# Optimization experiments

Measured on AMD Instinct MI355X. Metric: run time of the kernel, lower is better.

## Reference

```python
import jax, jax.numpy as jnp
import numpy as np

N = 50000
D = 1024
EPS = 1e-5

def gcn(x, W, b, src, dst, n):
    # PyG GCNConv: h = x @ W; add self-loops; symmetric normalization.
    h = x @ W
    deg = jnp.zeros((n,), h.dtype).at[dst].add(1.0) + 1.0  # +1 for self-loop
    dinv = jax.lax.rsqrt(deg)
    norm = dinv[src] * dinv[dst]                  # [E]
    agg = jnp.zeros_like(h).at[dst].add(h[src] * norm[:, None])
    agg = agg + h * (dinv * dinv)[:, None]        # self-loop contribution
    return agg + b

def bn(x, g, bt, m, v):
    # eval-mode BatchNorm1d with running stats
    return (x - m) * jax.lax.rsqrt(v + EPS) * g + bt

def branch(x, ei, W1, b1, g1, bt1, m1, v1, W2, b2, g2, bt2, m2, v2, W3, b3, g3, bt3, m3, v3):
    src, dst = ei[0], ei[1]
    h = jax.nn.relu(bn(gcn(x, W1, b1, src, dst, N), g1, bt1, m1, v1))
    h = jax.nn.relu(bn(gcn(h, W2, b2, src, dst, N), g2, bt2, m2, v2))
    emb = bn(gcn(h, W3, b3, src, dst, N), g3, bt3, m3, v3)   # node embeddings, no relu
    return jnp.mean(emb, axis=0, keepdims=True)              # [1, 64] global mean pool

def setup_inputs() -> dict:
    key = jax.random.key(0)
    ks = iter(jax.random.split(key, 64))
    inp = {}
    for i, nm in enumerate(['x0', 'x1', 'x2']):
        inp[nm] = jax.random.normal(next(ks), (N, D), jnp.float32)
    for nm, e in [('ei0', 150000), ('ei1', 300000), ('ei2', 600000)]:
        inp[nm] = jax.random.randint(next(ks), (2, e), 0, N, jnp.int64)
    dims = [(D, 256, '1'), (256, 128, '2'), (128, 64, '3')]
    for din, dout, s in dims:
        inp['W' + s + 's'] = jax.random.normal(next(ks), (3, din, dout), jnp.float32) * 0.02
        inp['B' + s + 's'] = jax.random.normal(next(ks), (3, dout), jnp.float32) * 0.02
        inp['g' + s + 's'] = jax.random.uniform(next(ks), (3, dout), jnp.float32, 0.5, 1.5)
        inp['bt' + s + 's'] = jax.random.normal(next(ks), (3, dout), jnp.float32) * 0.02
        inp['m' + s + 's'] = jax.random.normal(next(ks), (3, dout), jnp.float32) * 0.02
        inp['v' + s + 's'] = jax.random.uniform(next(ks), (3, dout), jnp.float32, 0.5, 1.5)
    inp['fuse_W'] = jax.random.normal(next(ks), (192, 64), jnp.float32) * 0.05
    inp['fuse_b'] = jax.random.normal(next(ks), (64,), jnp.float32) * 0.02
    inp['cls_W'] = jax.random.normal(next(ks), (64, 10), jnp.float32) * 0.1
    inp['cls_b'] = jax.random.normal(next(ks), (10,), jnp.float32) * 0.02
    inp['reg_W'] = jax.random.normal(next(ks), (64, 1), jnp.float32) * 0.1
    inp['reg_b'] = jax.random.normal(next(ks), (1,), jnp.float32) * 0.02
    return inp

def reference(x0, x1, x2, ei0, ei1, ei2,
              W1s, B1s, g1s, bt1s, m1s, v1s,
              W2s, B2s, g2s, bt2s, m2s, v2s,
              W3s, B3s, g3s, bt3s, m3s, v3s,
              fuse_W, fuse_b, cls_W, cls_b, reg_W, reg_b):
    xs = [x0, x1, x2]
    eis = [ei0, ei1, ei2]
    embs = []
    for s in range(3):  # fixed small loop over scales (different edge counts)
        embs.append(branch(xs[s], eis[s],
                           W1s[s], B1s[s], g1s[s], bt1s[s], m1s[s], v1s[s],
                           W2s[s], B2s[s], g2s[s], bt2s[s], m2s[s], v2s[s],
                           W3s[s], B3s[s], g3s[s], bt3s[s], m3s[s], v3s[s]))
    fused = jax.nn.relu(jnp.concatenate(embs, axis=-1) @ fuse_W + fuse_b)  # [1, 64]
    classification = fused @ cls_W + cls_b                                  # [1, 10]
    regression = jax.nn.sigmoid(fused @ reg_W + reg_b)                      # [1, 1]
    return (classification, regression)
```

## Files before the change

kernel.cpp:

```cpp
#include <hip/hip_runtime.h>
#include <cstdint>
#include <cstddef>

#define NNODES 50000

typedef __attribute__((ext_vector_type(8))) short short8;
typedef __attribute__((ext_vector_type(4))) float f32x4;
typedef __attribute__((ext_vector_type(4))) unsigned short u16x4;
typedef __attribute__((ext_vector_type(2))) unsigned short u16x2;
typedef __attribute__((ext_vector_type(4))) unsigned int u32x4;

__device__ __forceinline__ unsigned short f2bf(float f) {
  unsigned u = __builtin_bit_cast(unsigned, f);
  u = u + 0x7FFFu + ((u >> 16) & 1u);
  return (unsigned short)(u >> 16);
}
__device__ __forceinline__ float bf2f(unsigned short u) {
  return __builtin_bit_cast(float, (unsigned)u << 16);
}
__device__ __forceinline__ unsigned cvtpk(float lo, float hi) {
  unsigned r;
  asm("v_cvt_pk_bf16_f32 %0, %1, %2" : "=v"(r) : "v"(lo), "v"(hi));
  return r;
}

__global__ void deg_count3_kernel(const int* __restrict__ e0, const int* __restrict__ e1,
                                  const int* __restrict__ e2, int E0, int E1, int E2,
                                  int* __restrict__ deg, int n) {
  int s = blockIdx.y;
  const int* ei = s == 0 ? e0 : (s == 1 ? e1 : e2);
  int E = s == 0 ? E0 : (s == 1 ? E1 : E2);
  int i = blockIdx.x * blockDim.x + threadIdx.x;
  if (i < E) atomicAdd(&deg[(size_t)s * n + ei[E + i]], 1);
}

__global__ void deg_finish_kernel(const int* __restrict__ deg, float* __restrict__ dinv, int n) {
  int i = blockIdx.x * blockDim.x + threadIdx.x;
  if (i < n) dinv[i] = rsqrtf((float)deg[i] + 1.0f);
}

__global__ void csum_count3_kernel(const int* __restrict__ e0, const int* __restrict__ e1,
                                   const int* __restrict__ e2, int E0, int E1, int E2,
                                   const float* __restrict__ dinv_all, float* __restrict__ csum,
                                   int n) {
  int s = blockIdx.y;
  const int* ei = s == 0 ? e0 : (s == 1 ? e1 : e2);
  int E = s == 0 ? E0 : (s == 1 ? E1 : E2);
  int i = blockIdx.x * blockDim.x + threadIdx.x;
  if (i < E)
    unsafeAtomicAdd(&csum[(size_t)s * n + ei[i]], dinv_all[(size_t)s * n + ei[E + i]]);
}

__global__ void c_finish_kernel(const float* __restrict__ dinv, float* __restrict__ csum, int n) {
  int i = blockIdx.x * blockDim.x + threadIdx.x;
  if (i < n) csum[i] = dinv[i] * (dinv[i] + csum[i]);
}

__global__ void bsum_kernel(const int* __restrict__ deg, int* __restrict__ bsum, int n,
                            int nchunk) {
  int s = blockIdx.y, c = blockIdx.x;
  int i = c * 256 + threadIdx.x;
  int v = (i < n) ? deg[(size_t)s * n + i] : 0;
  __shared__ int red[256];
  red[threadIdx.x] = v;
  __syncthreads();
  for (int o = 128; o > 0; o >>= 1) {
    if (threadIdx.x < o) red[threadIdx.x] += red[threadIdx.x + o];
    __syncthreads();
  }
  if (threadIdx.x == 0) bsum[s * nchunk + c] = red[0];
}

__global__ void bscan_kernel(int* __restrict__ bsum, int nchunk) {
  int s = blockIdx.x;
  __shared__ int tmp[256];
  int v = (threadIdx.x < nchunk) ? bsum[s * nchunk + threadIdx.x] : 0;
  tmp[threadIdx.x] = v;
  __syncthreads();
  for (int o = 1; o < 256; o <<= 1) {
    int t = (threadIdx.x >= o) ? tmp[threadIdx.x - o] : 0;
    __syncthreads();
    tmp[threadIdx.x] += t;
    __syncthreads();
  }
  if (threadIdx.x < nchunk) bsum[s * nchunk + threadIdx.x] = tmp[threadIdx.x] - v;
}

__global__ void rowptr_kernel(const int* __restrict__ deg, const int* __restrict__ bsum,
                              int* __restrict__ rowptr, int* __restrict__ cursor, int n,
                              int nchunk) {
  int s = blockIdx.y, c = blockIdx.x;
  int i = c * 256 + threadIdx.x;
  int v = (i < n) ? deg[(size_t)s * n + i] : 0;
  __shared__ int tmp[256];
  tmp[threadIdx.x] = v;
  __syncthreads();
  for (int o = 1; o < 256; o <<= 1) {
    int t = (threadIdx.x >= o) ? tmp[threadIdx.x - o] : 0;
    __syncthreads();
    tmp[threadIdx.x] += t;
    __syncthreads();
  }
  int incl = tmp[threadIdx.x] + bsum[s * nchunk + c];
  if (i < n) {
    rowptr[(size_t)s * (n + 1) + i + 1] = incl;
    cursor[(size_t)s * n + i] = incl - v;
  }
  if (i == 0) rowptr[(size_t)s * (n + 1)] = 0;
}

__global__ void csr_fill3_kernel(const int* __restrict__ e0, const int* __restrict__ e1,
                                 const int* __restrict__ e2, int E0, int E1, int E2,
                                 int* __restrict__ cursor, int* __restrict__ csr, int n) {
  int s = blockIdx.y;
  const int* ei = s == 0 ? e0 : (s == 1 ? e1 : e2);
  int E = s == 0 ? E0 : (s == 1 ? E1 : E2);
  int coff = (s > 0 ? E0 : 0) + (s > 1 ? E1 : 0);
  int i = blockIdx.x * blockDim.x + threadIdx.x;
  if (i < E) {
    int src = ei[i];
    int dst = ei[E + i];
    int pos = atomicAdd(&cursor[(size_t)s * n + dst], 1);
    csr[coff + pos] = src;
  }
}

__global__ void wt_all_kernel(const float* __restrict__ W0, const float* __restrict__ W1,
                              unsigned short* __restrict__ Wt) {
  int idx = blockIdx.x * blockDim.x + threadIdx.x;
  const int L0TOT = 3 * 262144;
  const int TOT = L0TOT + 3 * 32768;
  if (idx >= TOT) return;
  if (idx < L0TOT) {
    int s = idx / 262144, r = idx - s * 262144;
    int n = r >> 10, k = r & 1023;
    Wt[idx] = f2bf(W0[(size_t)s * 262144 + k * 256 + n]);
  } else {
    int j = idx - L0TOT;
    int s = j / 32768, r = j - s * 32768;
    int n = r >> 8, k = r & 255;
    Wt[idx] = f2bf(W1[(size_t)s * 32768 + k * 128 + n]);
  }
}

template <int A_FP32, int WR, int WC, int NT>
__global__ __launch_bounds__(NT) void gemm_lds3_kernel(
    const void* __restrict__ A0v, const void* __restrict__ A1v, const void* __restrict__ A2v,
    const unsigned short* __restrict__ Wt, int wtStride,
    unsigned short* __restrict__ H, size_t hStride,
    const float* __restrict__ dinv_all, int M, int K, int Nc) {
  constexpr int BM = WR * 64;
  constexpr int BN = WC * 64;
  constexpr int ABYTES = BM * 64 * (A_FP32 ? 4 : 2);
  constexpr int BBYTES = BN * 64 * 2;
  constexpr int AISS = ABYTES / (16 * NT);
  constexpr int BISS = BBYTES / (16 * NT);

  __shared__ unsigned char lds[ABYTES + BBYTES];
  float* AldsF = (float*)lds;
  unsigned short* AldsH = (unsigned short*)lds;
  unsigned short* Blds = (unsigned short*)(lds + ABYTES);

  const int sc = blockIdx.y;
  const void* Av = sc == 0 ? A0v : (sc == 1 ? A1v : A2v);
  const unsigned short* Wts = Wt + (size_t)sc * wtStride;
  unsigned short* Hs = H + (size_t)sc * hStride;
  const float* dinv = dinv_all + (size_t)sc * M;
  const int tid = threadIdx.x;
  const int lane = tid & 63;
  const int w = tid >> 6;
  const int wr = w / WC;
  const int wc = w - wr * WC;
  const int r0 = blockIdx.x * BM;
  const float* Af = (const float*)Av;
  const unsigned short* Ab = (const unsigned short*)Av;
  const int NT16 = K >> 6;

  f32x4 acc[4][4] = {};

  for (int t = 0; t < NT16; ++t) {
    const int k0 = t << 6;
#pragma unroll
    for (int i = 0; i < AISS; i++) {
      int c = (w * AISS + i) * 64 + lane;
      if constexpr (A_FP32) {
        int row = c >> 4, j = c & 15;
        int gr = r0 + row;
        if (gr > M - 1) gr = M - 1;
        const float* src = Af + (size_t)gr * K + k0 + ((j ^ (row & 7)) << 2);
        __builtin_amdgcn_global_load_lds(
            (const __attribute__((address_space(1))) void*)src,
            (__attribute__((address_space(3))) void*)(lds + (size_t)(w * AISS + i) * 1024),
            16, 0, 0);
      } else {
        int row = c >> 3, j = c & 7;
        int gr = r0 + row;
        if (gr > M - 1) gr = M - 1;
        const unsigned short* src = Ab + (size_t)gr * K + k0 + ((j ^ (row & 7)) << 3);
        __builtin_amdgcn_global_load_lds(
            (const __attribute__((address_space(1))) void*)src,
            (__attribute__((address_space(3))) void*)(lds + (size_t)(w * AISS + i) * 1024),
            16, 0, 0);
      }
    }
#pragma unroll
    for (int i = 0; i < BISS; i++) {
      int c = (w * BISS + i) * 64 + lane;
      int n = c >> 3, j = c & 7;
      const unsigned short* src = Wts + (size_t)n * K + k0 + ((j ^ (n & 7)) << 3);
      __builtin_amdgcn_global_load_lds(
          (const __attribute__((address_space(1))) void*)src,
          (__attribute__((address_space(3))) void*)(lds + ABYTES + (size_t)(w * BISS + i) * 1024),
          16, 0, 0);
    }
    __syncthreads();

#pragma unroll
    for (int kk = 0; kk < 2; kk++) {
      const int t16 = kk * 4 + (lane >> 4);
      short8 af[4], bfr[4];
#pragma unroll
      for (int mi = 0; mi < 4; mi++) {
        int row = wr * 64 + mi * 16 + (lane & 15);
        if constexpr (A_FP32) {
          const float* bp = AldsF + row * 64;
          f32x4 u0 = *(const f32x4*)(bp + ((((2 * t16)) ^ (row & 7)) << 2));
          f32x4 u1 = *(const f32x4*)(bp + (((2 * t16 + 1) ^ (row & 7)) << 2));
          u32x4 p;
          p[0] = cvtpk(u0[0], u0[1]);
          p[1] = cvtpk(u0[2], u0[3]);
          p[2] = cvtpk(u1[0], u1[1]);
          p[3] = cvtpk(u1[2], u1[3]);
          af[mi] = __builtin_bit_cast(short8, p);
        } else {
          af[mi] = *(const short8*)(AldsH + row * 64 + ((t16 ^ (row & 7)) << 3));
        }
      }
#pragma unroll
      for (int ni = 0; ni < 4; ni++) {
        int n = wc * 64 + ni * 16 + (lane & 15);
        bfr[ni] = *(const short8*)(Blds + n * 64 + ((t16 ^ (n & 7)) << 3));
      }
#pragma unroll
      for (int mi = 0; mi < 4; mi++)
#pragma unroll
        for (int ni = 0; ni < 4; ni++)
          acc[mi][ni] =
              __builtin_amdgcn_mfma_f32_16x16x32_bf16(af[mi], bfr[ni], acc[mi][ni], 0, 0, 0);
    }
    __syncthreads();
  }

#pragma unroll
  for (int mi = 0; mi < 4; mi++) {
#pragma unroll
    for (int r = 0; r < 4; r++) {
      int gr = r0 + wr * 64 + mi * 16 + (lane >> 4) * 4 + r;
      if (gr < M) {
        float di = dinv[gr];
#pragma unroll
        for (int ni = 0; ni < 4; ni++) {
          int col = wc * 64 + ni * 16 + (lane & 15);
          Hs[(size_t)gr * Nc + col] = f2bf(acc[mi][ni][r] * di);
        }
      }
    }
  }
}

template <int VEC>
__device__ __forceinline__ void addrow(const unsigned short* __restrict__ p, float* acc) {
  if constexpr (VEC == 4) {
    u16x4 u = *(const u16x4*)p;
#pragma unroll
    for (int j = 0; j < 4; j++) acc[j] += bf2f(u[j]);
  } else {
    u16x2 u = *(const u16x2*)p;
    acc[0] += bf2f(u[0]);
    acc[1] += bf2f(u[1]);
  }
}

template <int VEC>
__global__ __launch_bounds__(256) void agg3_kernel(
    const unsigned short* __restrict__ Hb, size_t hStride,
    const int* __restrict__ rowptr, const int* __restrict__ csr, int E0, int E1,
    const float* __restrict__ dinv_all,
    const float* __restrict__ Bb, const float* __restrict__ g,
    const float* __restrict__ bt, const float* __restrict__ m,
    const float* __restrict__ v, unsigned short* __restrict__ X, size_t xStride, int n) {
  const int C = VEC * 64;
  const int sIdx = blockIdx.y;
  const unsigned short* Hs = Hb + (size_t)sIdx * hStride;
  unsigned short* Xs = X + (size_t)sIdx * xStride;
  const int* rp = rowptr + (size_t)sIdx * (n + 1);
  const int* cs = csr + (sIdx > 0 ? E0 : 0) + (sIdx > 1 ? E1 : 0);
  const float* dinv = dinv_all + (size_t)sIdx * n;
  const int lane = threadIdx.x & 63;
  const int w = threadIdx.x >> 6;
  const int ch = lane * VEC;
  float a[VEC], sh[VEC];
#pragma unroll
  for (int j = 0; j < VEC; j++) {
    float aa = g[sIdx * C + ch + j] * rsqrtf(v[sIdx * C + ch + j] + 1e-5f);
    a[j] = aa;
    sh[j] = (Bb[sIdx * C + ch + j] - m[sIdx * C + ch + j]) * aa + bt[sIdx * C + ch + j];
  }
  const int row = blockIdx.x * 4 + w;
  if (row >= n) return;
  float acc[VEC] = {};
  addrow<VEC>(Hs + (size_t)row * C + ch, acc);
  int b0 = rp[row], b1 = rp[row + 1];
  int i = b0;
  for (; i + 8 <= b1; i += 8) {
    int s0 = cs[i], s1 = cs[i + 1], s2 = cs[i + 2], s3 = cs[i + 3];
    int s4 = cs[i + 4], s5 = cs[i + 5], s6 = cs[i + 6], s7 = cs[i + 7];
    addrow<VEC>(Hs + (size_t)s0 * C + ch, acc);
    addrow<VEC>(Hs + (size_t)s1 * C + ch, acc);
    addrow<VEC>(Hs + (size_t)s2 * C + ch, acc);
    addrow<VEC>(Hs + (size_t)s3 * C + ch, acc);
    addrow<VEC>(Hs + (size_t)s4 * C + ch, acc);
    addrow<VEC>(Hs + (size_t)s5 * C + ch, acc);
    addrow<VEC>(Hs + (size_t)s6 * C + ch, acc);
    addrow<VEC>(Hs + (size_t)s7 * C + ch, acc);
  }
  for (; i < b1; i++) addrow<VEC>(Hs + (size_t)cs[i] * C + ch, acc);
  float dd = dinv[row];
  if constexpr (VEC == 4) {
    u16x4 o;
#pragma unroll
    for (int j = 0; j < 4; j++) o[j] = f2bf(fmaxf(acc[j] * dd * a[j] + sh[j], 0.0f));
    *(u16x4*)(Xs + (size_t)row * C + ch) = o;
  } else {
    u16x2 o;
    o[0] = f2bf(fmaxf(acc[0] * dd * a[0] + sh[0], 0.0f));
    o[1] = f2bf(fmaxf(acc[1] * dd * a[1] + sh[1], 0.0f));
    *(u16x2*)(Xs + (size_t)row * C + ch) = o;
  }
}

__global__ __launch_bounds__(256) void colsum3_kernel(const unsigned short* __restrict__ X,
                                                      size_t xStride,
                                                      const float* __restrict__ c_all,
                                                      float* __restrict__ pooled, int n) {
  const int s = blockIdx.y;
  const unsigned short* Xs = X + (size_t)s * xStride;
  const float* c = c_all + (size_t)s * n;
  const int ch = threadIdx.x & 127;
  const int half = threadIdx.x >> 7;
  float acc = 0.0f;
  for (int row = blockIdx.x * 2 + half; row < n; row += gridDim.x * 2)
    acc += c[row] * bf2f(Xs[(size_t)row * 128 + ch]);
  __shared__ float red[256];
  red[threadIdx.x] = acc;
  __syncthreads();
  if (threadIdx.x < 128)
    unsafeAtomicAdd(&pooled[s * 128 + ch], red[threadIdx.x] + red[threadIdx.x + 128]);
}

__global__ void head_kernel(const float* __restrict__ pooled, const float* __restrict__ W3p,
                            const float* __restrict__ B3p, const float* __restrict__ g3p,
                            const float* __restrict__ bt3p, const float* __restrict__ m3p,
                            const float* __restrict__ v3p, const float* __restrict__ fuse_W,
                            const float* __restrict__ fuse_b, const float* __restrict__ cls_W,
                            const float* __restrict__ cls_b, const float* __restrict__ reg_W,
                            const float* __restrict__ reg_b, float* __restrict__ out) {
  __shared__ float e[192];
  __shared__ float fused[64];
  int t = threadIdx.x;
  if (t < 192) {
    int s = t >> 6, ch = t & 63;
    float acc = 0.0f;
    const float* W3 = W3p + (size_t)s * 128 * 64;
    const float* pv = pooled + s * 128;
    for (int k = 0; k < 128; k++) acc += pv[k] * W3[k * 64 + ch];
    float a3 = g3p[s * 64 + ch] * rsqrtf(v3p[s * 64 + ch] + 1e-5f);
    e[t] = (acc * (1.0f / (float)NNODES) + B3p[s * 64 + ch] - m3p[s * 64 + ch]) * a3 +
           bt3p[s * 64 + ch];
  }
  __syncthreads();
  if (t < 64) {
    float acc = fuse_b[t];
    for (int k = 0; k < 192; k++) acc += e[k] * fuse_W[k * 64 + t];
    fused[t] = fmaxf(acc, 0.0f);
  }
  __syncthreads();
  if (t < 10) {
    float acc = cls_b[t];
    for (int k = 0; k < 64; k++) acc += fused[k] * cls_W[k * 10 + t];
    out[t] = acc;
  }
  if (t == 64) {
    float acc = reg_b[0];
    for (int k = 0; k < 64; k++) acc += fused[k] * reg_W[k];
    out[10] = 1.0f / (1.0f + expf(-acc));
  }
}

extern "C" void kernel_launch(void* const* d_in, const int* in_sizes, int n_in,
                              void* d_out, int out_size, void* d_ws, size_t ws_size,
                              hipStream_t stream) {
  const int N = NNODES;
  const int NCHUNK = (N + 255) / 256;
  const float* xs[3] = {(const float*)d_in[0], (const float*)d_in[1], (const float*)d_in[2]};
  const int* eis[3] = {(const int*)d_in[3], (const int*)d_in[4], (const int*)d_in[5]};
  int Es[3];
  for (int s = 0; s < 3; s++) Es[s] = in_sizes[3 + s] / 2;
  int maxE = Es[0] > Es[1] ? Es[0] : Es[1];
  if (Es[2] > maxE) maxE = Es[2];

  const float* Wp[2]  = {(const float*)d_in[6],  (const float*)d_in[12]};
  const float* Bp[2]  = {(const float*)d_in[7],  (const float*)d_in[13]};
  const float* gp[2]  = {(const float*)d_in[8],  (const float*)d_in[14]};
  const float* btp[2] = {(const float*)d_in[9],  (const float*)d_in[15]};
  const float* mp[2]  = {(const float*)d_in[10], (const float*)d_in[16]};
  const float* vp[2]  = {(const float*)d_in[11], (const float*)d_in[17]};
  const float* W3p  = (const float*)d_in[18];
  const float* B3p  = (const float*)d_in[19];
  const float* g3p  = (const float*)d_in[20];
  const float* bt3p = (const float*)d_in[21];
  const float* m3p  = (const float*)d_in[22];
  const float* v3p  = (const float*)d_in[23];
  const float* fuse_W = (const float*)d_in[24];
  const float* fuse_b = (const float*)d_in[25];
  const float* cls_W  = (const float*)d_in[26];
  const float* cls_b  = (const float*)d_in[27];
  const float* reg_W  = (const float*)d_in[28];
  const float* reg_b  = (const float*)d_in[29];

  size_t off = 0;
  auto alloc = [&](size_t nbytes) {
    char* p = (char*)d_ws + off;
    off += (nbytes + 255) & ~(size_t)255;
    return (void*)p;
  };
  int*   deg      = (int*)alloc(3 * (size_t)N * 4);
  float* dinv_all = (float*)alloc(3 * (size_t)N * 4);
  float* c_all    = (float*)alloc(3 * (size_t)N * 4);
  float* pooled   = (float*)alloc(3 * 128 * 4);
  int*   bsum     = (int*)alloc(3 * (size_t)NCHUNK * 4);
  int*   rowptr   = (int*)alloc(3 * (size_t)(N + 1) * 4);
  int*   cursor   = (int*)alloc(3 * (size_t)N * 4);
  int*   csr      = (int*)alloc((size_t)(Es[0] + Es[1] + Es[2]) * 4);
  unsigned short* Hbuf = (unsigned short*)alloc(3 * (size_t)N * 256 * 2);
  unsigned short* Xbf  = (unsigned short*)alloc(3 * (size_t)N * 256 * 2);
  unsigned short* Wt   = (unsigned short*)alloc((size_t)(3 * 262144 + 3 * 32768) * 2);
  (void)ws_size; (void)n_in; (void)out_size;

  const size_t HS = (size_t)N * 256;

  hipMemsetAsync(deg, 0, 3 * (size_t)N * 4, stream);
  hipMemsetAsync(c_all, 0, 3 * (size_t)N * 4, stream);
  hipMemsetAsync(pooled, 0, 3 * 128 * 4, stream);

  dim3 eg((maxE + 255) / 256, 3);
  deg_count3_kernel<<<eg, 256, 0, stream>>>(eis[0], eis[1], eis[2], Es[0], Es[1], Es[2], deg, N);
  deg_finish_kernel<<<(3 * N + 255) / 256, 256, 0, stream>>>(deg, dinv_all, 3 * N);
  csum_count3_kernel<<<eg, 256, 0, stream>>>(eis[0], eis[1], eis[2], Es[0], Es[1], Es[2],
                                             dinv_all, c_all, N);
  c_finish_kernel<<<(3 * N + 255) / 256, 256, 0, stream>>>(dinv_all, c_all, 3 * N);
  bsum_kernel<<<dim3(NCHUNK, 3), 256, 0, stream>>>(deg, bsum, N, NCHUNK);
  bscan_kernel<<<3, 256, 0, stream>>>(bsum, NCHUNK);
  rowptr_kernel<<<dim3(NCHUNK, 3), 256, 0, stream>>>(deg, bsum, rowptr, cursor, N, NCHUNK);
  csr_fill3_kernel<<<eg, 256, 0, stream>>>(eis[0], eis[1], eis[2], Es[0], Es[1], Es[2], cursor,
                                           csr, N);
  wt_all_kernel<<<(3 * 262144 + 3 * 32768 + 255) / 256, 256, 0, stream>>>(Wp[0], Wp[1], Wt);

  gemm_lds3_kernel<1, 2, 4, 512><<<dim3((N + 127) / 128, 3), 512, 0, stream>>>(
      xs[0], xs[1], xs[2], Wt, 262144, Hbuf, HS, dinv_all, N, 1024, 256);
  agg3_kernel<4><<<dim3((N + 3) / 4, 3), 256, 0, stream>>>(
      Hbuf, HS, rowptr, csr, Es[0], Es[1], dinv_all, Bp[0], gp[0], btp[0], mp[0], vp[0], Xbf,
      HS, N);

  gemm_lds3_kernel<0, 2, 2, 256><<<dim3((N + 127) / 128, 3), 256, 0, stream>>>(
      Xbf, Xbf + HS, Xbf + 2 * HS, Wt + 3 * 262144, 32768, Hbuf, HS, dinv_all, N, 256, 128);
  agg3_kernel<2><<<dim3((N + 3) / 4, 3), 256, 0, stream>>>(
      Hbuf, HS, rowptr, csr, Es[0], Es[1], dinv_all, Bp[1], gp[1], btp[1], mp[1], vp[1], Xbf,
      HS, N);

  colsum3_kernel<<<dim3(512, 3), 256, 0, stream>>>(Xbf, HS, c_all, pooled, N);

  head_kernel<<<1, 192, 0, stream>>>(pooled, W3p, B3p, g3p, bt3p, m3p, v3p, fuse_W, fuse_b,
                                     cls_W, cls_b, reg_W, reg_b, (float*)d_out);
}
```

Baseline: 712.5 us.

## Double-buffer LDS tiles in GEMM to overlap global loads with MFMA

```diff
diff --git a/kernel.cpp b/kernel.cpp
--- a/kernel.cpp
+++ b/kernel.cpp
@@ -143,23 +143,23 @@
   }
 }
 
-template <int A_FP32, int WR, int WC, int NT>
-__global__ __launch_bounds__(NT) void gemm_lds3_kernel(
+template <int A_FP32, int WR, int WC, int NT, int KDIM>
+__global__ __launch_bounds__(NT) void gemm_pipe3_kernel(
     const void* __restrict__ A0v, const void* __restrict__ A1v, const void* __restrict__ A2v,
     const unsigned short* __restrict__ Wt, int wtStride,
     unsigned short* __restrict__ H, size_t hStride,
-    const float* __restrict__ dinv_all, int M, int K, int Nc) {
+    const float* __restrict__ dinv_all, int M, int Nc) {
   constexpr int BM = WR * 64;
   constexpr int BN = WC * 64;
   constexpr int ABYTES = BM * 64 * (A_FP32 ? 4 : 2);
   constexpr int BBYTES = BN * 64 * 2;
+  constexpr int TILEB = ABYTES + BBYTES;
   constexpr int AISS = ABYTES / (16 * NT);
   constexpr int BISS = BBYTES / (16 * NT);
-
-  __shared__ unsigned char lds[ABYTES + BBYTES];
-  float* AldsF = (float*)lds;
-  unsigned short* AldsH = (unsigned short*)lds;
-  unsigned short* Blds = (unsigned short*)(lds + ABYTES);
+  constexpr int ISS = AISS + BISS;
+  constexpr int NTILES = KDIM / 64;
+
+  __shared__ unsigned char lds[2 * TILEB];
 
   const int sc = blockIdx.y;
   const void* Av = sc == 0 ? A0v : (sc == 1 ? A1v : A2v);
@@ -174,12 +174,10 @@
   const int r0 = blockIdx.x * BM;
   const float* Af = (const float*)Av;
   const unsigned short* Ab = (const unsigned short*)Av;
-  const int NT16 = K >> 6;
-
-  f32x4 acc[4][4] = {};
-
-  for (int t = 0; t < NT16; ++t) {
+
+  auto issueTile = [&](int t, int buf) {
     const int k0 = t << 6;
+    unsigned char* ldsb = lds + (size_t)buf * TILEB;
 #pragma unroll
     for (int i = 0; i < AISS; i++) {
       int c = (w * AISS + i) * 64 + lane;
@@ -187,19 +185,19 @@
         int row = c >> 4, j = c & 15;
         int gr = r0 + row;
         if (gr > M - 1) gr = M - 1;
-        const float* src = Af + (size_t)gr * K + k0 + ((j ^ (row & 7)) << 2);
+        const float* src = Af + (size_t)gr * KDIM + k0 + ((j ^ (row & 7)) << 2);
         __builtin_amdgcn_global_load_lds(
             (const __attribute__((address_space(1))) void*)src,
-            (__attribute__((address_space(3))) void*)(lds + (size_t)(w * AISS + i) * 1024),
+            (__attribute__((address_space(3))) void*)(ldsb + (size_t)(w * AISS + i) * 1024),
             16, 0, 0);
       } else {
         int row = c >> 3, j = c & 7;
         int gr = r0 + row;
         if (gr > M - 1) gr = M - 1;
-        const unsigned short* src = Ab + (size_t)gr * K + k0 + ((j ^ (row & 7)) << 3);
+        const unsigned short* src = Ab + (size_t)gr * KDIM + k0 + ((j ^ (row & 7)) << 3);
         __builtin_amdgcn_global_load_lds(
             (const __attribute__((address_space(1))) void*)src,
-            (__attribute__((address_space(3))) void*)(lds + (size_t)(w * AISS + i) * 1024),
+            (__attribute__((address_space(3))) void*)(ldsb + (size_t)(w * AISS + i) * 1024),
             16, 0, 0);
       }
     }
@@ -207,14 +205,22 @@
     for (int i = 0; i < BISS; i++) {
       int c = (w * BISS + i) * 64 + lane;
       int n = c >> 3, j = c & 7;
-      const unsigned short* src = Wts + (size_t)n * K + k0 + ((j ^ (n & 7)) << 3);
+      const unsigned short* src = Wts + (size_t)n * KDIM + k0 + ((j ^ (n & 7)) << 3);
       __builtin_amdgcn_global_load_lds(
           (const __attribute__((address_space(1))) void*)src,
-          (__attribute__((address_space(3))) void*)(lds + ABYTES + (size_t)(w * BISS + i) * 1024),
+          (__attribute__((address_space(3))) void*)(ldsb + ABYTES +
+                                                    (size_t)(w * BISS + i) * 1024),
           16, 0, 0);
     }
-    __syncthreads();
-
+  };
+
+  f32x4 acc[4][4] = {};
+
+  auto computeT = [&](int buf) {
+    const float* AldsF = (const float*)(lds + (size_t)buf * TILEB);
+    const unsigned short* AldsH = (const unsigned short*)(lds + (size_t)buf * TILEB);
+    const unsigned short* Blds =
+        (const unsigned short*)(lds + (size_t)buf * TILEB + ABYTES);
 #pragma unroll
     for (int kk = 0; kk < 2; kk++) {
       const int t16 = kk * 4 + (lane >> 4);
@@ -248,8 +254,21 @@
           acc[mi][ni] =
               __builtin_amdgcn_mfma_f32_16x16x32_bf16(af[mi], bfr[ni], acc[mi][ni], 0, 0, 0);
     }
-    __syncthreads();
-  }
+  };
+
+  issueTile(0, 0);
+  issueTile(1, 1);
+#pragma unroll 1
+  for (int t = 0; t < NTILES - 1; ++t) {
+    asm volatile("s_waitcnt vmcnt(%0)" ::"n"(ISS) : "memory");
+    asm volatile("s_barrier" ::: "memory");
+    computeT(t & 1);
+    asm volatile("s_waitcnt lgkmcnt(0)\ns_barrier" ::: "memory");
+    if (t + 2 < NTILES) issueTile(t + 2, t & 1);
+  }
+  asm volatile("s_waitcnt vmcnt(0)" ::: "memory");
+  asm volatile("s_barrier" ::: "memory");
+  computeT((NTILES - 1) & 1);
 
 #pragma unroll
   for (int mi = 0; mi < 4; mi++) {
@@ -466,14 +485,14 @@
                                            csr, N);
   wt_all_kernel<<<(3 * 262144 + 3 * 32768 + 255) / 256, 256, 0, stream>>>(Wp[0], Wp[1], Wt);
 
-  gemm_lds3_kernel<1, 2, 4, 512><<<dim3((N + 127) / 128, 3), 512, 0, stream>>>(
-      xs[0], xs[1], xs[2], Wt, 262144, Hbuf, HS, dinv_all, N, 1024, 256);
+  gemm_pipe3_kernel<1, 2, 4, 512, 1024><<<dim3((N + 127) / 128, 3), 512, 0, stream>>>(
+      xs[0], xs[1], xs[2], Wt, 262144, Hbuf, HS, dinv_all, N, 256);
   agg3_kernel<4><<<dim3((N + 3) / 4, 3), 256, 0, stream>>>(
       Hbuf, HS, rowptr, csr, Es[0], Es[1], dinv_all, Bp[0], gp[0], btp[0], mp[0], vp[0], Xbf,
       HS, N);
 
-  gemm_lds3_kernel<0, 2, 2, 256><<<dim3((N + 127) / 128, 3), 256, 0, stream>>>(
-      Xbf, Xbf + HS, Xbf + 2 * HS, Wt + 3 * 262144, 32768, Hbuf, HS, dinv_all, N, 256, 128);
+  gemm_pipe3_kernel<0, 2, 2, 256, 256><<<dim3((N + 127) / 128, 3), 256, 0, stream>>>(
+      Xbf, Xbf + HS, Xbf + 2 * HS, Wt + 3 * 262144, 32768, Hbuf, HS, dinv_all, N, 128);
   agg3_kernel<2><<<dim3((N + 3) / 4, 3), 256, 0, stream>>>(
       Hbuf, HS, rowptr, csr, Es[0], Es[1], dinv_all, Bp[1], gp[1], btp[1], mp[1], vp[1], Xbf,
       HS, N);
```

New measurement: 676.5 us. 1.05x faster.

## Fuse weighted column-sum pooling into layer-2 aggregation and retile first GEMM

Applied to the files above, without the earlier changes.

```diff
diff --git a/kernel.cpp b/kernel.cpp
--- a/kernel.cpp
+++ b/kernel.cpp
@@ -281,14 +281,15 @@
   }
 }
 
-template <int VEC>
+template <int VEC, int POOL>
 __global__ __launch_bounds__(256) void agg3_kernel(
     const unsigned short* __restrict__ Hb, size_t hStride,
     const int* __restrict__ rowptr, const int* __restrict__ csr, int E0, int E1,
     const float* __restrict__ dinv_all,
     const float* __restrict__ Bb, const float* __restrict__ g,
     const float* __restrict__ bt, const float* __restrict__ m,
-    const float* __restrict__ v, unsigned short* __restrict__ X, size_t xStride, int n) {
+    const float* __restrict__ v, unsigned short* __restrict__ X, size_t xStride,
+    const float* __restrict__ c_all, float* __restrict__ pooled_rep, int n) {
   const int C = VEC * 64;
   const int sIdx = blockIdx.y;
   const unsigned short* Hs = Hb + (size_t)sIdx * hStride;
@@ -296,6 +297,7 @@
   const int* rp = rowptr + (size_t)sIdx * (n + 1);
   const int* cs = csr + (sIdx > 0 ? E0 : 0) + (sIdx > 1 ? E1 : 0);
   const float* dinv = dinv_all + (size_t)sIdx * n;
+  const float* cw = c_all + (size_t)sIdx * n;
   const int lane = threadIdx.x & 63;
   const int w = threadIdx.x >> 6;
   const int ch = lane * VEC;
@@ -306,74 +308,83 @@
     a[j] = aa;
     sh[j] = (Bb[sIdx * C + ch + j] - m[sIdx * C + ch + j]) * aa + bt[sIdx * C + ch + j];
   }
-  const int row = blockIdx.x * 4 + w;
-  if (row >= n) return;
-  float acc[VEC] = {};
-  addrow<VEC>(Hs + (size_t)row * C + ch, acc);
-  int b0 = rp[row], b1 = rp[row + 1];
-  int i = b0;
-  for (; i + 8 <= b1; i += 8) {
-    int s0 = cs[i], s1 = cs[i + 1], s2 = cs[i + 2], s3 = cs[i + 3];
-    int s4 = cs[i + 4], s5 = cs[i + 5], s6 = cs[i + 6], s7 = cs[i + 7];
-    addrow<VEC>(Hs + (size_t)s0 * C + ch, acc);
-    addrow<VEC>(Hs + (size_t)s1 * C + ch, acc);
-    addrow<VEC>(Hs + (size_t)s2 * C + ch, acc);
-    addrow<VEC>(Hs + (size_t)s3 * C + ch, acc);
-    addrow<VEC>(Hs + (size_t)s4 * C + ch, acc);
-    addrow<VEC>(Hs + (size_t)s5 * C + ch, acc);
-    addrow<VEC>(Hs + (size_t)s6 * C + ch, acc);
-    addrow<VEC>(Hs + (size_t)s7 * C + ch, acc);
-  }
-  for (; i < b1; i++) addrow<VEC>(Hs + (size_t)cs[i] * C + ch, acc);
-  float dd = dinv[row];
-  if constexpr (VEC == 4) {
-    u16x4 o;
-#pragma unroll
-    for (int j = 0; j < 4; j++) o[j] = f2bf(fmaxf(acc[j] * dd * a[j] + sh[j], 0.0f));
-    *(u16x4*)(Xs + (size_t)row * C + ch) = o;
-  } else {
-    u16x2 o;
-    o[0] = f2bf(fmaxf(acc[0] * dd * a[0] + sh[0], 0.0f));
-    o[1] = f2bf(fmaxf(acc[1] * dd * a[1] + sh[1], 0.0f));
-    *(u16x2*)(Xs + (size_t)row * C + ch) = o;
-  }
-}
-
-__global__ __launch_bounds__(256) void colsum3_kernel(const unsigned short* __restrict__ X,
-                                                      size_t xStride,
-                                                      const float* __restrict__ c_all,
-                                                      float* __restrict__ pooled, int n) {
-  const int s = blockIdx.y;
-  const unsigned short* Xs = X + (size_t)s * xStride;
-  const float* c = c_all + (size_t)s * n;
-  const int ch = threadIdx.x & 127;
-  const int half = threadIdx.x >> 7;
-  float acc = 0.0f;
-  for (int row = blockIdx.x * 2 + half; row < n; row += gridDim.x * 2)
-    acc += c[row] * bf2f(Xs[(size_t)row * 128 + ch]);
-  __shared__ float red[256];
-  red[threadIdx.x] = acc;
-  __syncthreads();
-  if (threadIdx.x < 128)
-    unsafeAtomicAdd(&pooled[s * 128 + ch], red[threadIdx.x] + red[threadIdx.x + 128]);
-}
-
-__global__ void head_kernel(const float* __restrict__ pooled, const float* __restrict__ W3p,
+  float pool[VEC] = {};
+  const int stride = gridDim.x * 4;
+  for (int row = blockIdx.x * 4 + w; row < n; row += stride) {
+    float acc[VEC] = {};
+    addrow<VEC>(Hs + (size_t)row * C + ch, acc);
+    int b0 = rp[row], b1 = rp[row + 1];
+    int i = b0;
+    for (; i + 8 <= b1; i += 8) {
+      int s0 = cs[i], s1 = cs[i + 1], s2 = cs[i + 2], s3 = cs[i + 3];
+      int s4 = cs[i + 4], s5 = cs[i + 5], s6 = cs[i + 6], s7 = cs[i + 7];
+      addrow<VEC>(Hs + (size_t)s0 * C + ch, acc);
+      addrow<VEC>(Hs + (size_t)s1 * C + ch, acc);
+      addrow<VEC>(Hs + (size_t)s2 * C + ch, acc);
+      addrow<VEC>(Hs + (size_t)s3 * C + ch, acc);
+      addrow<VEC>(Hs + (size_t)s4 * C + ch, acc);
+      addrow<VEC>(Hs + (size_t)s5 * C + ch, acc);
+      addrow<VEC>(Hs + (size_t)s6 * C + ch, acc);
+      addrow<VEC>(Hs + (size_t)s7 * C + ch, acc);
+    }
+    for (; i < b1; i++) addrow<VEC>(Hs + (size_t)cs[i] * C + ch, acc);
+    float dd = dinv[row];
+    if constexpr (!POOL) {
+      if constexpr (VEC == 4) {
+        u16x4 o;
+#pragma unroll
+        for (int j = 0; j < 4; j++) o[j] = f2bf(fmaxf(acc[j] * dd * a[j] + sh[j], 0.0f));
+        *(u16x4*)(Xs + (size_t)row * C + ch) = o;
+      } else {
+        u16x2 o;
+        o[0] = f2bf(fmaxf(acc[0] * dd * a[0] + sh[0], 0.0f));
+        o[1] = f2bf(fmaxf(acc[1] * dd * a[1] + sh[1], 0.0f));
+        *(u16x2*)(Xs + (size_t)row * C + ch) = o;
+      }
+    } else {
+      float cr = cw[row];
+#pragma unroll
+      for (int j = 0; j < VEC; j++)
+        pool[j] += cr * fmaxf(acc[j] * dd * a[j] + sh[j], 0.0f);
+    }
+  }
+  if constexpr (POOL) {
+    __shared__ float red[4 * 128];
+#pragma unroll
+    for (int j = 0; j < VEC; j++) red[w * 128 + ch + j] = pool[j];
+    __syncthreads();
+    int t = threadIdx.x;
+    if (t < 128) {
+      float val = red[t] + red[128 + t] + red[256 + t] + red[384 + t];
+      unsafeAtomicAdd(&pooled_rep[(((size_t)(blockIdx.x & 7) * 3 + sIdx) << 7) + t], val);
+    }
+  }
+}
+
+__global__ void head_kernel(const float* __restrict__ pooled_rep, const float* __restrict__ W3p,
                             const float* __restrict__ B3p, const float* __restrict__ g3p,
                             const float* __restrict__ bt3p, const float* __restrict__ m3p,
                             const float* __restrict__ v3p, const float* __restrict__ fuse_W,
                             const float* __restrict__ fuse_b, const float* __restrict__ cls_W,
                             const float* __restrict__ cls_b, const float* __restrict__ reg_W,
                             const float* __restrict__ reg_b, float* __restrict__ out) {
+  __shared__ float pv[3 * 128];
   __shared__ float e[192];
   __shared__ float fused[64];
   int t = threadIdx.x;
+  for (int idx = t; idx < 384; idx += 192) {
+    int s = idx >> 7, k = idx & 127;
+    float acc = 0.0f;
+#pragma unroll
+    for (int r = 0; r < 8; r++) acc += pooled_rep[((r * 3 + s) << 7) + k];
+    pv[idx] = acc;
+  }
+  __syncthreads();
   if (t < 192) {
     int s = t >> 6, ch = t & 63;
     float acc = 0.0f;
     const float* W3 = W3p + (size_t)s * 128 * 64;
-    const float* pv = pooled + s * 128;
-    for (int k = 0; k < 128; k++) acc += pv[k] * W3[k * 64 + ch];
+    for (int k = 0; k < 128; k++) acc += pv[s * 128 + k] * W3[k * 64 + ch];
     float a3 = g3p[s * 64 + ch] * rsqrtf(v3p[s * 64 + ch] + 1e-5f);
     e[t] = (acc * (1.0f / (float)NNODES) + B3p[s * 64 + ch] - m3p[s * 64 + ch]) * a3 +
            bt3p[s * 64 + ch];
@@ -434,14 +445,14 @@
     off += (nbytes + 255) & ~(size_t)255;
     return (void*)p;
   };
-  int*   deg      = (int*)alloc(3 * (size_t)N * 4);
-  float* dinv_all = (float*)alloc(3 * (size_t)N * 4);
-  float* c_all    = (float*)alloc(3 * (size_t)N * 4);
-  float* pooled   = (float*)alloc(3 * 128 * 4);
-  int*   bsum     = (int*)alloc(3 * (size_t)NCHUNK * 4);
-  int*   rowptr   = (int*)alloc(3 * (size_t)(N + 1) * 4);
-  int*   cursor   = (int*)alloc(3 * (size_t)N * 4);
-  int*   csr      = (int*)alloc((size_t)(Es[0] + Es[1] + Es[2]) * 4);
+  int*   deg        = (int*)alloc(3 * (size_t)N * 4);
+  float* dinv_all   = (float*)alloc(3 * (size_t)N * 4);
+  float* c_all      = (float*)alloc(3 * (size_t)N * 4);
+  float* pooled_rep = (float*)alloc(8 * 3 * 128 * 4);
+  int*   bsum       = (int*)alloc(3 * (size_t)NCHUNK * 4);
+  int*   rowptr     = (int*)alloc(3 * (size_t)(N + 1) * 4);
+  int*   cursor     = (int*)alloc(3 * (size_t)N * 4);
+  int*   csr        = (int*)alloc((size_t)(Es[0] + Es[1] + Es[2]) * 4);
   unsigned short* Hbuf = (unsigned short*)alloc(3 * (size_t)N * 256 * 2);
   unsigned short* Xbf  = (unsigned short*)alloc(3 * (size_t)N * 256 * 2);
   unsigned short* Wt   = (unsigned short*)alloc((size_t)(3 * 262144 + 3 * 32768) * 2);
@@ -451,7 +462,7 @@
 
   hipMemsetAsync(deg, 0, 3 * (size_t)N * 4, stream);
   hipMemsetAsync(c_all, 0, 3 * (size_t)N * 4, stream);
-  hipMemsetAsync(pooled, 0, 3 * 128 * 4, stream);
+  hipMemsetAsync(pooled_rep, 0, 8 * 3 * 128 * 4, stream);
 
   dim3 eg((maxE + 255) / 256, 3);
   deg_count3_kernel<<<eg, 256, 0, stream>>>(eis[0], eis[1], eis[2], Es[0], Es[1], Es[2], deg, N);
@@ -466,20 +477,18 @@
                                            csr, N);
   wt_all_kernel<<<(3 * 262144 + 3 * 32768 + 255) / 256, 256, 0, stream>>>(Wp[0], Wp[1], Wt);
 
-  gemm_lds3_kernel<1, 2, 4, 512><<<dim3((N + 127) / 128, 3), 512, 0, stream>>>(
+  gemm_lds3_kernel<1, 1, 4, 256><<<dim3((N + 63) / 64, 3), 256, 0, stream>>>(
       xs[0], xs[1], xs[2], Wt, 262144, Hbuf, HS, dinv_all, N, 1024, 256);
-  agg3_kernel<4><<<dim3((N + 3) / 4, 3), 256, 0, stream>>>(
+  agg3_kernel<4, 0><<<dim3((N + 15) / 16, 3), 256, 0, stream>>>(
       Hbuf, HS, rowptr, csr, Es[0], Es[1], dinv_all, Bp[0], gp[0], btp[0], mp[0], vp[0], Xbf,
-      HS, N);
+      HS, c_all, pooled_rep, N);
 
   gemm_lds3_kernel<0, 2, 2, 256><<<dim3((N + 127) / 128, 3), 256, 0, stream>>>(
       Xbf, Xbf + HS, Xbf + 2 * HS, Wt + 3 * 262144, 32768, Hbuf, HS, dinv_all, N, 256, 128);
-  agg3_kernel<2><<<dim3((N + 3) / 4, 3), 256, 0, stream>>>(
+  agg3_kernel<2, 1><<<dim3((N + 15) / 16, 3), 256, 0, stream>>>(
       Hbuf, HS, rowptr, csr, Es[0], Es[1], dinv_all, Bp[1], gp[1], btp[1], mp[1], vp[1], Xbf,
-      HS, N);
-
-  colsum3_kernel<<<dim3(512, 3), 256, 0, stream>>>(Xbf, HS, c_all, pooled, N);
-
-  head_kernel<<<1, 192, 0, stream>>>(pooled, W3p, B3p, g3p, bt3p, m3p, v3p, fuse_W, fuse_b,
+      HS, c_all, pooled_rep, N);
+
+  head_kernel<<<1, 192, 0, stream>>>(pooled_rep, W3p, B3p, g3p, bt3p, m3p, v3p, fuse_W, fuse_b,
                                      cls_W, cls_b, reg_W, reg_b, (float*)d_out);
 }
```

Result: faster. 622.7 us (-12.6%).
